# Optimization experiments

Measured on AMD Instinct MI355X. Metric: run time of the kernel, lower is better.

## Reference

```python
import jax, jax.numpy as jnp
import numpy as np

N = 10000   # nodes
E = 320000  # directed edges (self-loops added inside reference, per PyG default)
H1, C = 4, 128  # gat1: 4 heads x 128; gat2: 1 head x 128
NEG_SLOPE = 0.2


def _glorot(k, shape):
    lim = float(np.sqrt(6.0 / (shape[0] + shape[-1])))
    return jax.random.uniform(k, shape, jnp.float32, -lim, lim)


def setup_inputs() -> dict:
    key = jax.random.key(0)
    ks = jax.random.split(key, 12)
    x = jax.random.normal(ks[0], (N, 2), jnp.float32)
    edge_index = jax.random.randint(ks[1], (2, E), 0, N, dtype=jnp.int32).astype(jnp.int64)
    W1 = _glorot(ks[2], (2, H1 * C))
    att_src1 = _glorot(ks[3], (H1, C))
    att_dst1 = _glorot(ks[4], (H1, C))
    b1 = jnp.zeros((H1 * C,), jnp.float32)
    W2 = _glorot(ks[5], (H1 * C, C))
    att_src2 = _glorot(ks[6], (1, C))
    att_dst2 = _glorot(ks[7], (1, C))
    b2 = jnp.zeros((C,), jnp.float32)
    Wp = _glorot(ks[8], (C, 1))
    bp = jnp.zeros((1,), jnp.float32)
    return dict(x=x, edge_index=edge_index, W1=W1, att_src1=att_src1, att_dst1=att_dst1,
                b1=b1, W2=W2, att_src2=att_src2, att_dst2=att_dst2, b2=b2, Wp=Wp, bp=bp)


def _gat_conv(x, src, dst, W, a_src, a_dst, b, heads, ch, concat):
    n = x.shape[0]
    h = (x @ W).reshape(n, heads, ch)                         # [N,H,C]
    # per-node attention halves, gathered per edge
    e = jax.nn.leaky_relu((h * a_src).sum(-1)[src] + (h * a_dst).sum(-1)[dst],
                          NEG_SLOPE)                           # [E,H]
    # segment softmax over incoming edges of each destination node
    m = jax.ops.segment_max(e, dst, num_segments=n)            # [N,H]
    p = jnp.exp(e - m[dst])
    s = jax.ops.segment_sum(p, dst, num_segments=n)
    alpha = p / (s[dst] + 1e-16)                               # [E,H]
    out = jax.ops.segment_sum(h[src] * alpha[..., None], dst, num_segments=n)  # [N,H,C]
    out = out.reshape(n, heads * ch) if concat else out.mean(axis=1)
    return out + b


def reference(x, edge_index, W1, att_src1, att_dst1, b1, W2, att_src2, att_dst2, b2, Wp, bp):
    n = x.shape[0]
    loop = jnp.arange(n, dtype=edge_index.dtype)               # PyG add_self_loops=True
    src = jnp.concatenate([edge_index[0], loop])
    dst = jnp.concatenate([edge_index[1], loop])
    h = jax.nn.relu(_gat_conv(x, src, dst, W1, att_src1, att_dst1, b1, H1, C, True))
    h = jax.nn.relu(_gat_conv(h, src, dst, W2, att_src2, att_dst2, b2, 1, C, True))
    logits = h @ Wp + bp                                       # [N,1]
    return logits.squeeze(-1)
```

## Files before the change

### kernel.cpp

```cpp
#include <hip/hip_runtime.h>
#include <math.h>

#define N_NODES 10000
#define E_IN    320000
#define E_TOT   330000
#define H1      4
#define C       128
#define F1      512
#define CAP     1024

__global__ __launch_bounds__(512) void k_prep(
    const float* __restrict__ W1, const float* __restrict__ asw,
    const float* __restrict__ adw, float* __restrict__ prep)
{
    int j = threadIdx.x;
    float w0 = W1[j], w1 = W1[F1 + j];
    float a = asw[j], d = adw[j];
    float p0 = w0 * a, p1 = w1 * a, q0 = w0 * d, q1 = w1 * d;
    #pragma unroll
    for (int o = 32; o > 0; o >>= 1) {
        p0 += __shfl_down(p0, o); p1 += __shfl_down(p1, o);
        q0 += __shfl_down(q0, o); q1 += __shfl_down(q1, o);
    }
    __shared__ float red[8][4];
    int wave = j >> 6, lane = j & 63;
    if (lane == 0) { red[wave][0] = p0; red[wave][1] = p1; red[wave][2] = q0; red[wave][3] = q1; }
    __syncthreads();
    if (j < 4) {
        prep[j]      = red[2*j][0] + red[2*j+1][0];
        prep[4 + j]  = red[2*j][1] + red[2*j+1][1];
        prep[8 + j]  = red[2*j][2] + red[2*j+1][2];
        prep[12 + j] = red[2*j][3] + red[2*j+1][3];
    }
}

__global__ void k_as1z(const float* __restrict__ x, const float* __restrict__ prep,
                       float4* __restrict__ as1v, float4* __restrict__ ad1v,
                       int* __restrict__ deg)
{
    int n = blockIdx.x * blockDim.x + threadIdx.x;
    if (n >= N_NODES) return;
    deg[n] = 0;
    float x0 = x[2*n], x1 = x[2*n+1];
    float4 A0 = *(const float4*)(prep);
    float4 A1 = *(const float4*)(prep + 4);
    float4 D0 = *(const float4*)(prep + 8);
    float4 D1 = *(const float4*)(prep + 12);
    as1v[n] = make_float4(x0*A0.x + x1*A1.x, x0*A0.y + x1*A1.y,
                          x0*A0.z + x1*A1.z, x0*A0.w + x1*A1.w);
    ad1v[n] = make_float4(x0*D0.x + x1*D1.x, x0*D0.y + x1*D1.y,
                          x0*D0.z + x1*D1.z, x0*D0.w + x1*D1.w);
}

__global__ void k_hist(const int* __restrict__ dsti, int* __restrict__ deg) {
    int t = blockIdx.x * blockDim.x + threadIdx.x;
    if (t >= E_TOT) return;
    int d = (t < E_IN) ? dsti[t] : (t - E_IN);
    atomicAdd(&deg[d], 1);
}

__global__ __launch_bounds__(256) void k_scan(
    const int* __restrict__ deg, int* __restrict__ offs, int* __restrict__ cursor)
{
    __shared__ int part[256];
    int tid = threadIdx.x;
    const int CH = (N_NODES + 255) / 256;
    int start = tid * CH;
    int sum = 0;
    for (int i = 0; i < CH; ++i) { int idx = start + i; if (idx < N_NODES) sum += deg[idx]; }
    part[tid] = sum;
    __syncthreads();
    for (int off = 1; off < 256; off <<= 1) {
        int v = (tid >= off) ? part[tid - off] : 0;
        __syncthreads();
        part[tid] += v;
        __syncthreads();
    }
    int base = (tid == 0) ? 0 : part[tid - 1];
    for (int i = 0; i < CH; ++i) {
        int idx = start + i;
        if (idx < N_NODES) { offs[idx] = base; cursor[idx] = base; base += deg[idx]; }
    }
    if (tid == 255) offs[N_NODES] = base;
}

__global__ void k_scatter(const int* __restrict__ srci, const int* __restrict__ dsti,
                          int* __restrict__ cursor, int* __restrict__ scsr) {
    int t = blockIdx.x * blockDim.x + threadIdx.x;
    if (t >= E_TOT) return;
    int d = (t < E_IN) ? dsti[t] : (t - E_IN);
    int s = (t < E_IN) ? srci[t] : (t - E_IN);
    int pos = atomicAdd(&cursor[d], 1);
    scsr[pos] = s;
}

__global__ __launch_bounds__(256) void k_fused1(
    const int* __restrict__ offs, const int* __restrict__ scsr,
    const float4* __restrict__ as1v, const float4* __restrict__ ad1v,
    const float2* __restrict__ xv, float* __restrict__ wxn)
{
    int node = blockIdx.x * 4 + (threadIdx.x >> 6);
    int lane = threadIdx.x & 63;
    if (node >= N_NODES) return;
    int beg = offs[node], end = offs[node + 1];
    float4 ad = ad1v[node];
    float s0 = 0.f, s1 = 0.f, s2 = 0.f, s3 = 0.f;
    float w00 = 0.f, w01 = 0.f, w10 = 0.f, w11 = 0.f;
    float w20 = 0.f, w21 = 0.f, w30 = 0.f, w31 = 0.f;
    for (int i = beg + lane; i < end; i += 64) {
        int s = scsr[i];
        float4 a = as1v[s];
        float2 xs = xv[s];
        float e0 = a.x + ad.x; e0 = e0 > 0.f ? e0 : 0.2f*e0;
        float e1 = a.y + ad.y; e1 = e1 > 0.f ? e1 : 0.2f*e1;
        float e2 = a.z + ad.z; e2 = e2 > 0.f ? e2 : 0.2f*e2;
        float e3 = a.w + ad.w; e3 = e3 > 0.f ? e3 : 0.2f*e3;
        float p0 = __expf(e0), p1 = __expf(e1), p2 = __expf(e2), p3 = __expf(e3);
        s0 += p0; s1 += p1; s2 += p2; s3 += p3;
        w00 += p0*xs.x; w01 += p0*xs.y; w10 += p1*xs.x; w11 += p1*xs.y;
        w20 += p2*xs.x; w21 += p2*xs.y; w30 += p3*xs.x; w31 += p3*xs.y;
    }
    #pragma unroll
    for (int o = 1; o < 64; o <<= 1) {
        s0 += __shfl_xor(s0, o); s1 += __shfl_xor(s1, o);
        s2 += __shfl_xor(s2, o); s3 += __shfl_xor(s3, o);
        w00 += __shfl_xor(w00, o); w01 += __shfl_xor(w01, o);
        w10 += __shfl_xor(w10, o); w11 += __shfl_xor(w11, o);
        w20 += __shfl_xor(w20, o); w21 += __shfl_xor(w21, o);
        w30 += __shfl_xor(w30, o); w31 += __shfl_xor(w31, o);
    }
    if (lane == 0) {
        float i0 = 1.f/(s0 + 1e-16f), i1 = 1.f/(s1 + 1e-16f);
        float i2 = 1.f/(s2 + 1e-16f), i3 = 1.f/(s3 + 1e-16f);
        float4* W = (float4*)(wxn + node*8);
        W[0] = make_float4(w00*i0, w01*i0, w10*i1, w11*i1);
        W[1] = make_float4(w20*i2, w21*i2, w30*i3, w31*i3);
    }
}

__global__ __launch_bounds__(256) void k_gemm2(
    const float* __restrict__ wxn, const float* __restrict__ W1,
    const float* __restrict__ b1, const float* __restrict__ W2,
    const float* __restrict__ asw, const float* __restrict__ adw,
    float* __restrict__ h2, float* __restrict__ as2, float* __restrict__ ad2)
{
    __shared__ float A_lds[64][16];
    __shared__ float B_lds[64 * C];
    __shared__ float wls[16 * 8];
    int n0 = blockIdx.x * 16;
    int tid = threadIdx.x;
    int cg = tid & 31;
    int ng = tid >> 5;
    if (tid < 128) wls[tid] = wxn[n0*8 + tid];

    float acc0x = 0.f, acc0y = 0.f, acc0z = 0.f, acc0w = 0.f;
    float acc1x = 0.f, acc1y = 0.f, acc1z = 0.f, acc1w = 0.f;

    int kl = tid >> 2;
    int nq = (tid & 3) * 4;

    for (int kc = 0; kc < 8; ++kc) {
        __syncthreads();
        const float* Wsrc = W2 + kc * (64 * C);
        #pragma unroll
        for (int i = tid * 4; i < 64 * C; i += 1024)
            *(float4*)(B_lds + i) = *(const float4*)(Wsrc + i);
        {
            int kg = kc * 64 + kl;
            int h2i = (kc >> 1) * 2;
            float w1a = W1[kg], w1b = W1[F1 + kg], bb = b1[kg];
            #pragma unroll
            for (int u = 0; u < 4; ++u) {
                int n = nq + u;
                float v = wls[n*8 + h2i] * w1a + wls[n*8 + h2i + 1] * w1b + bb;
                A_lds[kl][n] = v > 0.f ? v : 0.f;
            }
        }
        __syncthreads();
        #pragma unroll 8
        for (int k = 0; k < 64; ++k) {
            float2 a = *(const float2*)&A_lds[k][2*ng];
            float4 b = *(const float4*)&B_lds[k*C + 4*cg];
            acc0x += a.x*b.x; acc0y += a.x*b.y; acc0z += a.x*b.z; acc0w += a.x*b.w;
            acc1x += a.y*b.x; acc1y += a.y*b.y; acc1z += a.y*b.z; acc1w += a.y*b.w;
        }
    }
    int r0 = n0 + 2*ng;
    *(float4*)(h2 + (size_t)r0*C + 4*cg)     = make_float4(acc0x, acc0y, acc0z, acc0w);
    *(float4*)(h2 + (size_t)(r0+1)*C + 4*cg) = make_float4(acc1x, acc1y, acc1z, acc1w);
    float4 av = *(const float4*)(asw + 4*cg);
    float4 dv = *(const float4*)(adw + 4*cg);
    float ps0 = acc0x*av.x + acc0y*av.y + acc0z*av.z + acc0w*av.w;
    float pd0 = acc0x*dv.x + acc0y*dv.y + acc0z*dv.z + acc0w*dv.w;
    float ps1 = acc1x*av.x + acc1y*av.y + acc1z*av.z + acc1w*av.w;
    float pd1 = acc1x*dv.x + acc1y*dv.y + acc1z*dv.z + acc1w*dv.w;
    #pragma unroll
    for (int o = 1; o < 32; o <<= 1) {
        ps0 += __shfl_xor(ps0, o); pd0 += __shfl_xor(pd0, o);
        ps1 += __shfl_xor(ps1, o); pd1 += __shfl_xor(pd1, o);
    }
    if (cg == 0) {
        as2[r0] = ps0; ad2[r0] = pd0;
        as2[r0+1] = ps1; ad2[r0+1] = pd1;
    }
}

__global__ __launch_bounds__(128) void k_agg2(
    const int* __restrict__ offs, const int* __restrict__ scsr,
    const float* __restrict__ as2, const float* __restrict__ ad2,
    const float* __restrict__ h2, const float* __restrict__ b2,
    const float* __restrict__ Wp, const float* __restrict__ bp,
    float* __restrict__ out)
{
    __shared__ float p_lds[CAP];
    __shared__ int   s_lds[CAP];
    __shared__ float red[2];
    int n = blockIdx.x, tid = threadIdx.x;
    int beg = offs[n], end = offs[n + 1];
    int degn = end - beg;
    int cnt = degn < CAP ? degn : CAP;
    float adn = ad2[n];
    float psum = 0.f;
    for (int j = tid; j < cnt; j += 128) {
        int s = scsr[beg + j];
        float e = as2[s] + adn; e = e > 0.f ? e : 0.2f*e;
        float p = __expf(e);
        p_lds[j] = p; s_lds[j] = s;
        psum += p;
    }
    for (int j = CAP + tid; j < degn; j += 128) {
        int s = scsr[beg + j];
        float e = as2[s] + adn; e = e > 0.f ? e : 0.2f*e;
        psum += __expf(e);
    }
    #pragma unroll
    for (int o = 32; o > 0; o >>= 1) psum += __shfl_down(psum, o);
    if ((tid & 63) == 0) red[tid >> 6] = psum;
    __syncthreads();
    float inv = 1.f / (red[0] + red[1] + 1e-16f);
    int c = tid;
    float acc = 0.f;
    for (int j = 0; j < cnt; ++j)
        acc += p_lds[j] * h2[(size_t)s_lds[j]*C + c];
    for (int j = CAP; j < degn; ++j) {
        int s = scsr[beg + j];
        float e = as2[s] + adn; e = e > 0.f ? e : 0.2f*e;
        acc += __expf(e) * h2[(size_t)s*C + c];
    }
    float v = acc * inv + b2[c];
    v = v > 0.f ? v : 0.f;
    float contrib = v * Wp[c];
    #pragma unroll
    for (int o = 32; o > 0; o >>= 1) contrib += __shfl_down(contrib, o);
    __syncthreads();
    if ((tid & 63) == 0) red[tid >> 6] = contrib;
    __syncthreads();
    if (tid == 0) out[n] = red[0] + red[1] + bp[0];
}

extern "C" void kernel_launch(void* const* d_in, const int* in_sizes, int n_in,
                              void* d_out, int out_size, void* d_ws, size_t ws_size,
                              hipStream_t stream)
{
    const float* x    = (const float*)d_in[0];
    const int*   ei   = (const int*)d_in[1];
    const int*   srci = ei;
    const int*   dsti = ei + E_IN;
    const float* W1   = (const float*)d_in[2];
    const float* as1w = (const float*)d_in[3];
    const float* ad1w = (const float*)d_in[4];
    const float* b1   = (const float*)d_in[5];
    const float* W2   = (const float*)d_in[6];
    const float* as2w = (const float*)d_in[7];
    const float* ad2w = (const float*)d_in[8];
    const float* b2   = (const float*)d_in[9];
    const float* Wp   = (const float*)d_in[10];
    const float* bp   = (const float*)d_in[11];
    float* out = (float*)d_out;

    char* ws = (char*)d_ws;
    size_t off = 0;
    auto alloc = [&](size_t bytes) -> char* {
        char* p = ws + off;
        off = (off + bytes + 255) & ~(size_t)255;
        return p;
    };
    float*  prep   = (float*)alloc(16 * 4);
    float4* as1v   = (float4*)alloc((size_t)N_NODES * 16);
    float4* ad1v   = (float4*)alloc((size_t)N_NODES * 16);
    float*  wxn    = (float*)alloc((size_t)N_NODES * 8 * 4);
    float*  h2     = (float*)alloc((size_t)N_NODES * C * 4);
    float*  as2    = (float*)alloc((size_t)N_NODES * 4);
    float*  ad2    = (float*)alloc((size_t)N_NODES * 4);
    int*    deg    = (int*)alloc((size_t)N_NODES * 4);
    int*    offs   = (int*)alloc((size_t)(N_NODES + 1) * 4);
    int*    cursor = (int*)alloc((size_t)N_NODES * 4);
    int*    scsr   = (int*)alloc((size_t)E_TOT * 4);

    const int EB = 256;
    const int egrid = (E_TOT + EB - 1) / EB;
    const int ngrid = (N_NODES + 255) / 256;

    k_prep<<<1, 512, 0, stream>>>(W1, as1w, ad1w, prep);
    k_as1z<<<ngrid, 256, 0, stream>>>(x, prep, as1v, ad1v, deg);

    k_hist<<<egrid, EB, 0, stream>>>(dsti, deg);
    k_scan<<<1, 256, 0, stream>>>(deg, offs, cursor);
    k_scatter<<<egrid, EB, 0, stream>>>(srci, dsti, cursor, scsr);

    k_fused1<<<(N_NODES + 3) / 4, 256, 0, stream>>>(offs, scsr, as1v, ad1v,
                                                    (const float2*)x, wxn);

    k_gemm2<<<N_NODES / 16, 256, 0, stream>>>(wxn, W1, b1, W2, as2w, ad2w, h2, as2, ad2);
    k_agg2<<<N_NODES, 128, 0, stream>>>(offs, scsr, as2, ad2, h2, b2, Wp, bp, out);
}
```

Measured before the change: 218.4 us.

## Fuse prep into node kernel, store h2 in fp16, slim agg2 and fused1 mapping

Folds the one-block attention-weight precompute into every block of k_as1z, removing one launch. k_fused1 now uses 16 lanes per node instead of a full wave, since average degree is about 33. h2 is stored as fp16 to halve gather traffic in layer-2 aggregation. k_agg2 becomes a single 64-lane wave that loops serially over edges with half2 loads, with no LDS staging. The fp16 storage of h2 lowers precision.

```diff
diff --git a/kernel.cpp b/kernel.cpp
--- a/kernel.cpp
+++ b/kernel.cpp
@@ -1,4 +1,5 @@
 #include <hip/hip_runtime.h>
+#include <hip/hip_fp16.h>
 #include <math.h>
 
 #define N_NODES 10000
@@ -7,45 +8,53 @@
 #define H1      4
 #define C       128
 #define F1      512
-#define CAP     1024
-
-__global__ __launch_bounds__(512) void k_prep(
-    const float* __restrict__ W1, const float* __restrict__ asw,
-    const float* __restrict__ adw, float* __restrict__ prep)
-{
-    int j = threadIdx.x;
-    float w0 = W1[j], w1 = W1[F1 + j];
-    float a = asw[j], d = adw[j];
-    float p0 = w0 * a, p1 = w1 * a, q0 = w0 * d, q1 = w1 * d;
-    #pragma unroll
-    for (int o = 32; o > 0; o >>= 1) {
-        p0 += __shfl_down(p0, o); p1 += __shfl_down(p1, o);
-        q0 += __shfl_down(q0, o); q1 += __shfl_down(q1, o);
-    }
-    __shared__ float red[8][4];
-    int wave = j >> 6, lane = j & 63;
-    if (lane == 0) { red[wave][0] = p0; red[wave][1] = p1; red[wave][2] = q0; red[wave][3] = q1; }
-    __syncthreads();
-    if (j < 4) {
-        prep[j]      = red[2*j][0] + red[2*j+1][0];
-        prep[4 + j]  = red[2*j][1] + red[2*j+1][1];
-        prep[8 + j]  = red[2*j][2] + red[2*j+1][2];
-        prep[12 + j] = red[2*j][3] + red[2*j+1][3];
-    }
-}
-
-__global__ void k_as1z(const float* __restrict__ x, const float* __restrict__ prep,
-                       float4* __restrict__ as1v, float4* __restrict__ ad1v,
-                       int* __restrict__ deg)
-{
-    int n = blockIdx.x * blockDim.x + threadIdx.x;
+
+__global__ __launch_bounds__(256) void k_as1z(
+    const float* __restrict__ x, const float* __restrict__ W1,
+    const float* __restrict__ asw, const float* __restrict__ adw,
+    float4* __restrict__ as1v, float4* __restrict__ ad1v, int* __restrict__ deg)
+{
+    __shared__ float red[4][8];
+    __shared__ float prep_s[16];
+    int tid = threadIdx.x;
+    {
+        int j = tid;
+        int j2 = tid + 256;
+        float w0a = W1[j],  w1a = W1[F1 + j];
+        float w0b = W1[j2], w1b = W1[F1 + j2];
+        float aa = asw[j], dd = adw[j], ab = asw[j2], db = adw[j2];
+        float q0 = w0a*aa, q1 = w1a*aa, q2 = w0a*dd, q3 = w1a*dd;
+        float q4 = w0b*ab, q5 = w1b*ab, q6 = w0b*db, q7 = w1b*db;
+        #pragma unroll
+        for (int o = 32; o > 0; o >>= 1) {
+            q0 += __shfl_down(q0, o); q1 += __shfl_down(q1, o);
+            q2 += __shfl_down(q2, o); q3 += __shfl_down(q3, o);
+            q4 += __shfl_down(q4, o); q5 += __shfl_down(q5, o);
+            q6 += __shfl_down(q6, o); q7 += __shfl_down(q7, o);
+        }
+        int wave = tid >> 6, lane = tid & 63;
+        if (lane == 0) {
+            red[wave][0] = q0; red[wave][1] = q1; red[wave][2] = q2; red[wave][3] = q3;
+            red[wave][4] = q4; red[wave][5] = q5; red[wave][6] = q6; red[wave][7] = q7;
+        }
+        __syncthreads();
+        if (tid < 16) {
+            int t = tid >> 2;
+            int h = tid & 3;
+            int w0 = (h & 1) * 2;
+            int r  = t + (h >> 1) * 4;
+            prep_s[t*4 + h] = red[w0][r] + red[w0+1][r];
+        }
+        __syncthreads();
+    }
+    int n = blockIdx.x * 256 + tid;
     if (n >= N_NODES) return;
     deg[n] = 0;
     float x0 = x[2*n], x1 = x[2*n+1];
-    float4 A0 = *(const float4*)(prep);
-    float4 A1 = *(const float4*)(prep + 4);
-    float4 D0 = *(const float4*)(prep + 8);
-    float4 D1 = *(const float4*)(prep + 12);
+    float4 A0 = *(const float4*)(prep_s);
+    float4 A1 = *(const float4*)(prep_s + 4);
+    float4 D0 = *(const float4*)(prep_s + 8);
+    float4 D1 = *(const float4*)(prep_s + 12);
     as1v[n] = make_float4(x0*A0.x + x1*A1.x, x0*A0.y + x1*A1.y,
                           x0*A0.z + x1*A1.z, x0*A0.w + x1*A1.w);
     ad1v[n] = make_float4(x0*D0.x + x1*D1.x, x0*D0.y + x1*D1.y,
@@ -99,15 +108,14 @@
     const float4* __restrict__ as1v, const float4* __restrict__ ad1v,
     const float2* __restrict__ xv, float* __restrict__ wxn)
 {
-    int node = blockIdx.x * 4 + (threadIdx.x >> 6);
-    int lane = threadIdx.x & 63;
-    if (node >= N_NODES) return;
+    int node = blockIdx.x * 16 + (threadIdx.x >> 4);
+    int sub = threadIdx.x & 15;
     int beg = offs[node], end = offs[node + 1];
     float4 ad = ad1v[node];
     float s0 = 0.f, s1 = 0.f, s2 = 0.f, s3 = 0.f;
     float w00 = 0.f, w01 = 0.f, w10 = 0.f, w11 = 0.f;
     float w20 = 0.f, w21 = 0.f, w30 = 0.f, w31 = 0.f;
-    for (int i = beg + lane; i < end; i += 64) {
+    for (int i = beg + sub; i < end; i += 16) {
         int s = scsr[i];
         float4 a = as1v[s];
         float2 xs = xv[s];
@@ -121,7 +129,7 @@
         w20 += p2*xs.x; w21 += p2*xs.y; w30 += p3*xs.x; w31 += p3*xs.y;
     }
     #pragma unroll
-    for (int o = 1; o < 64; o <<= 1) {
+    for (int o = 1; o < 16; o <<= 1) {
         s0 += __shfl_xor(s0, o); s1 += __shfl_xor(s1, o);
         s2 += __shfl_xor(s2, o); s3 += __shfl_xor(s3, o);
         w00 += __shfl_xor(w00, o); w01 += __shfl_xor(w01, o);
@@ -129,7 +137,7 @@
         w20 += __shfl_xor(w20, o); w21 += __shfl_xor(w21, o);
         w30 += __shfl_xor(w30, o); w31 += __shfl_xor(w31, o);
     }
-    if (lane == 0) {
+    if (sub == 0) {
         float i0 = 1.f/(s0 + 1e-16f), i1 = 1.f/(s1 + 1e-16f);
         float i2 = 1.f/(s2 + 1e-16f), i3 = 1.f/(s3 + 1e-16f);
         float4* W = (float4*)(wxn + node*8);
@@ -142,120 +150,102 @@
     const float* __restrict__ wxn, const float* __restrict__ W1,
     const float* __restrict__ b1, const float* __restrict__ W2,
     const float* __restrict__ asw, const float* __restrict__ adw,
-    float* __restrict__ h2, float* __restrict__ as2, float* __restrict__ ad2)
-{
-    __shared__ float A_lds[64][16];
+    __half* __restrict__ h2h, float* __restrict__ as2, float* __restrict__ ad2)
+{
     __shared__ float B_lds[64 * C];
-    __shared__ float wls[16 * 8];
+    __shared__ float A_lds[64 * 16];
+    __shared__ float wls[16 * 9];
+    int tid = threadIdx.x;
     int n0 = blockIdx.x * 16;
-    int tid = threadIdx.x;
+    if (tid < 128) {
+        int n = tid >> 3, q = tid & 7;
+        wls[n*9 + q] = wxn[(n0 + n)*8 + q];
+    }
     int cg = tid & 31;
     int ng = tid >> 5;
-    if (tid < 128) wls[tid] = wxn[n0*8 + tid];
-
-    float acc0x = 0.f, acc0y = 0.f, acc0z = 0.f, acc0w = 0.f;
-    float acc1x = 0.f, acc1y = 0.f, acc1z = 0.f, acc1w = 0.f;
-
-    int kl = tid >> 2;
-    int nq = (tid & 3) * 4;
+    int e_n = tid & 15, e_kq = tid >> 4;
+    float acc00 = 0.f, acc01 = 0.f, acc02 = 0.f, acc03 = 0.f;
+    float acc10 = 0.f, acc11 = 0.f, acc12 = 0.f, acc13 = 0.f;
 
     for (int kc = 0; kc < 8; ++kc) {
         __syncthreads();
         const float* Wsrc = W2 + kc * (64 * C);
         #pragma unroll
-        for (int i = tid * 4; i < 64 * C; i += 1024)
-            *(float4*)(B_lds + i) = *(const float4*)(Wsrc + i);
-        {
-            int kg = kc * 64 + kl;
-            int h2i = (kc >> 1) * 2;
-            float w1a = W1[kg], w1b = W1[F1 + kg], bb = b1[kg];
-            #pragma unroll
-            for (int u = 0; u < 4; ++u) {
-                int n = nq + u;
-                float v = wls[n*8 + h2i] * w1a + wls[n*8 + h2i + 1] * w1b + bb;
-                A_lds[kl][n] = v > 0.f ? v : 0.f;
-            }
+        for (int i = 0; i < 8; ++i)
+            *(float4*)(B_lds + tid*4 + i*1024) = *(const float4*)(Wsrc + tid*4 + i*1024);
+        int h2i = (kc >> 1) * 2;
+        float wa = wls[e_n*9 + h2i], wb = wls[e_n*9 + h2i + 1];
+        #pragma unroll
+        for (int u = 0; u < 4; ++u) {
+            int kl = e_kq*4 + u;
+            int kg = kc*64 + kl;
+            float v = wa * W1[kg] + wb * W1[F1 + kg] + b1[kg];
+            A_lds[kl*16 + e_n] = v > 0.f ? v : 0.f;
         }
         __syncthreads();
         #pragma unroll 8
         for (int k = 0; k < 64; ++k) {
-            float2 a = *(const float2*)&A_lds[k][2*ng];
-            float4 b = *(const float4*)&B_lds[k*C + 4*cg];
-            acc0x += a.x*b.x; acc0y += a.x*b.y; acc0z += a.x*b.z; acc0w += a.x*b.w;
-            acc1x += a.y*b.x; acc1y += a.y*b.y; acc1z += a.y*b.z; acc1w += a.y*b.w;
+            float2 a = *(const float2*)(A_lds + k*16 + 2*ng);
+            float4 b = *(const float4*)(B_lds + k*C + 4*cg);
+            acc00 += a.x*b.x; acc01 += a.x*b.y; acc02 += a.x*b.z; acc03 += a.x*b.w;
+            acc10 += a.y*b.x; acc11 += a.y*b.y; acc12 += a.y*b.z; acc13 += a.y*b.w;
         }
     }
     int r0 = n0 + 2*ng;
-    *(float4*)(h2 + (size_t)r0*C + 4*cg)     = make_float4(acc0x, acc0y, acc0z, acc0w);
-    *(float4*)(h2 + (size_t)(r0+1)*C + 4*cg) = make_float4(acc1x, acc1y, acc1z, acc1w);
+    {
+        __half2 lo0 = __floats2half2_rn(acc00, acc01);
+        __half2 hi0 = __floats2half2_rn(acc02, acc03);
+        __half2 lo1 = __floats2half2_rn(acc10, acc11);
+        __half2 hi1 = __floats2half2_rn(acc12, acc13);
+        *(uint2*)(h2h + (size_t)r0*C + 4*cg)     = make_uint2(*(uint*)&lo0, *(uint*)&hi0);
+        *(uint2*)(h2h + (size_t)(r0+1)*C + 4*cg) = make_uint2(*(uint*)&lo1, *(uint*)&hi1);
+    }
     float4 av = *(const float4*)(asw + 4*cg);
     float4 dv = *(const float4*)(adw + 4*cg);
-    float ps0 = acc0x*av.x + acc0y*av.y + acc0z*av.z + acc0w*av.w;
-    float pd0 = acc0x*dv.x + acc0y*dv.y + acc0z*dv.z + acc0w*dv.w;
-    float ps1 = acc1x*av.x + acc1y*av.y + acc1z*av.z + acc1w*av.w;
-    float pd1 = acc1x*dv.x + acc1y*dv.y + acc1z*dv.z + acc1w*dv.w;
+    float ps0 = acc00*av.x + acc01*av.y + acc02*av.z + acc03*av.w;
+    float pd0 = acc00*dv.x + acc01*dv.y + acc02*dv.z + acc03*dv.w;
+    float ps1 = acc10*av.x + acc11*av.y + acc12*av.z + acc13*av.w;
+    float pd1 = acc10*dv.x + acc11*dv.y + acc12*dv.z + acc13*dv.w;
     #pragma unroll
     for (int o = 1; o < 32; o <<= 1) {
         ps0 += __shfl_xor(ps0, o); pd0 += __shfl_xor(pd0, o);
         ps1 += __shfl_xor(ps1, o); pd1 += __shfl_xor(pd1, o);
     }
     if (cg == 0) {
-        as2[r0] = ps0; ad2[r0] = pd0;
+        as2[r0] = ps0;   ad2[r0] = pd0;
         as2[r0+1] = ps1; ad2[r0+1] = pd1;
     }
 }
 
-__global__ __launch_bounds__(128) void k_agg2(
+__global__ __launch_bounds__(64) void k_agg2(
     const int* __restrict__ offs, const int* __restrict__ scsr,
     const float* __restrict__ as2, const float* __restrict__ ad2,
-    const float* __restrict__ h2, const float* __restrict__ b2,
+    const __half* __restrict__ h2h, const float* __restrict__ b2,
     const float* __restrict__ Wp, const float* __restrict__ bp,
     float* __restrict__ out)
 {
-    __shared__ float p_lds[CAP];
-    __shared__ int   s_lds[CAP];
-    __shared__ float red[2];
-    int n = blockIdx.x, tid = threadIdx.x;
+    int n = blockIdx.x, lane = threadIdx.x;
     int beg = offs[n], end = offs[n + 1];
-    int degn = end - beg;
-    int cnt = degn < CAP ? degn : CAP;
     float adn = ad2[n];
-    float psum = 0.f;
-    for (int j = tid; j < cnt; j += 128) {
-        int s = scsr[beg + j];
+    float accx = 0.f, accy = 0.f, psum = 0.f;
+    for (int i = beg; i < end; ++i) {
+        int s = scsr[i];
         float e = as2[s] + adn; e = e > 0.f ? e : 0.2f*e;
         float p = __expf(e);
-        p_lds[j] = p; s_lds[j] = s;
         psum += p;
-    }
-    for (int j = CAP + tid; j < degn; j += 128) {
-        int s = scsr[beg + j];
-        float e = as2[s] + adn; e = e > 0.f ? e : 0.2f*e;
-        psum += __expf(e);
-    }
+        __half2 hv = *(const __half2*)(h2h + (size_t)s*C + 2*lane);
+        float2 f = __half22float2(hv);
+        accx += p * f.x; accy += p * f.y;
+    }
+    float inv = 1.f / (psum + 1e-16f);
+    float2 bb = *(const float2*)(b2 + 2*lane);
+    float2 wp = *(const float2*)(Wp + 2*lane);
+    float v0 = accx*inv + bb.x; v0 = v0 > 0.f ? v0 : 0.f;
+    float v1 = accy*inv + bb.y; v1 = v1 > 0.f ? v1 : 0.f;
+    float contrib = v0*wp.x + v1*wp.y;
     #pragma unroll
-    for (int o = 32; o > 0; o >>= 1) psum += __shfl_down(psum, o);
-    if ((tid & 63) == 0) red[tid >> 6] = psum;
-    __syncthreads();
-    float inv = 1.f / (red[0] + red[1] + 1e-16f);
-    int c = tid;
-    float acc = 0.f;
-    for (int j = 0; j < cnt; ++j)
-        acc += p_lds[j] * h2[(size_t)s_lds[j]*C + c];
-    for (int j = CAP; j < degn; ++j) {
-        int s = scsr[beg + j];
-        float e = as2[s] + adn; e = e > 0.f ? e : 0.2f*e;
-        acc += __expf(e) * h2[(size_t)s*C + c];
-    }
-    float v = acc * inv + b2[c];
-    v = v > 0.f ? v : 0.f;
-    float contrib = v * Wp[c];
-    #pragma unroll
-    for (int o = 32; o > 0; o >>= 1) contrib += __shfl_down(contrib, o);
-    __syncthreads();
-    if ((tid & 63) == 0) red[tid >> 6] = contrib;
-    __syncthreads();
-    if (tid == 0) out[n] = red[0] + red[1] + bp[0];
+    for (int o = 1; o < 64; o <<= 1) contrib += __shfl_xor(contrib, o);
+    if (lane == 0) out[n] = contrib + bp[0];
 }
 
 extern "C" void kernel_launch(void* const* d_in, const int* in_sizes, int n_in,
@@ -285,11 +275,10 @@
         off = (off + bytes + 255) & ~(size_t)255;
         return p;
     };
-    float*  prep   = (float*)alloc(16 * 4);
     float4* as1v   = (float4*)alloc((size_t)N_NODES * 16);
     float4* ad1v   = (float4*)alloc((size_t)N_NODES * 16);
     float*  wxn    = (float*)alloc((size_t)N_NODES * 8 * 4);
-    float*  h2     = (float*)alloc((size_t)N_NODES * C * 4);
+    __half* h2h    = (__half*)alloc((size_t)N_NODES * C * 2);
     float*  as2    = (float*)alloc((size_t)N_NODES * 4);
     float*  ad2    = (float*)alloc((size_t)N_NODES * 4);
     int*    deg    = (int*)alloc((size_t)N_NODES * 4);
@@ -301,16 +290,12 @@
     const int egrid = (E_TOT + EB - 1) / EB;
     const int ngrid = (N_NODES + 255) / 256;
 
-    k_prep<<<1, 512, 0, stream>>>(W1, as1w, ad1w, prep);
-    k_as1z<<<ngrid, 256, 0, stream>>>(x, prep, as1v, ad1v, deg);
-
+    k_as1z<<<ngrid, 256, 0, stream>>>(x, W1, as1w, ad1w, as1v, ad1v, deg);
     k_hist<<<egrid, EB, 0, stream>>>(dsti, deg);
     k_scan<<<1, 256, 0, stream>>>(deg, offs, cursor);
     k_scatter<<<egrid, EB, 0, stream>>>(srci, dsti, cursor, scsr);
-
-    k_fused1<<<(N_NODES + 3) / 4, 256, 0, stream>>>(offs, scsr, as1v, ad1v,
-                                                    (const float2*)x, wxn);
-
-    k_gemm2<<<N_NODES / 16, 256, 0, stream>>>(wxn, W1, b1, W2, as2w, ad2w, h2, as2, ad2);
-    k_agg2<<<N_NODES, 128, 0, stream>>>(offs, scsr, as2, ad2, h2, b2, Wp, bp, out);
-}
+    k_fused1<<<N_NODES / 16, 256, 0, stream>>>(offs, scsr, as1v, ad1v,
+                                               (const float2*)x, wxn);
+    k_gemm2<<<N_NODES / 16, 256, 0, stream>>>(wxn, W1, b1, W2, as2w, ad2w, h2h, as2, ad2);
+    k_agg2<<<N_NODES, 64, 0, stream>>>(offs, scsr, as2, ad2, h2h, b2, Wp, bp, out);
+}
```

Measured after the change: 217.8 us. About the same (-0.3%).
